# Kernel tuning notes

Measured on AMD Instinct MI355X. Metric: run time of the kernel, lower is better.

## Reference

```python
import jax, jax.numpy as jnp
import numpy as np
from jax import lax

K = 3
STRIDE = 1
PAD = 1
DIL = 1
EPS = 1e-5


def conv2d(x, w, b):
    y = lax.conv_general_dilated(
        x, w, (STRIDE, STRIDE), [(PAD, PAD), (PAD, PAD)],
        rhs_dilation=(DIL, DIL), dimension_numbers=('NCHW', 'OIHW', 'NCHW'))
    return y + b[None, :, None, None]


def deform_conv(x, offset, w):
    # x: [B,C,H,W], offset: [B,2*K2,Ho,Wo] (dy,dx interleaved per tap), w: [O,C,K,K]
    B, C, H, W = x.shape
    O = w.shape[0]
    K2 = K * K
    Ho, Wo = offset.shape[2], offset.shape[3]
    ky, kx = jnp.meshgrid(jnp.arange(K), jnp.arange(K), indexing='ij')
    # base sampling grid per kernel tap: [K2,Ho,Wo] (broadcast)
    by = (ky.reshape(K2, 1, 1) * DIL).astype(x.dtype) + (jnp.arange(Ho) * STRIDE - PAD).astype(x.dtype).reshape(1, Ho, 1)
    bx = (kx.reshape(K2, 1, 1) * DIL).astype(x.dtype) + (jnp.arange(Wo) * STRIDE - PAD).astype(x.dtype).reshape(1, 1, Wo)
    off = offset.reshape(B, K2, 2, Ho, Wo)
    py = by[None] + off[:, :, 0]  # [B,K2,Ho,Wo]
    px = bx[None] + off[:, :, 1]
    y0 = jnp.floor(py)
    x0 = jnp.floor(px)
    wy = py - y0
    wx = px - x0
    y0i = y0.astype(jnp.int32)
    x0i = x0.astype(jnp.int32)
    x_flat = x.reshape(B, C, H * W)

    def corner(yi, xi, cw):
        valid = ((yi >= 0) & (yi < H) & (xi >= 0) & (xi < W)).astype(x.dtype)
        idx = (jnp.clip(yi, 0, H - 1) * W + jnp.clip(xi, 0, W - 1)).reshape(B, -1)
        v = jax.vmap(lambda xb, ib: xb[:, ib])(x_flat, idx)  # [B,C,K2*Ho*Wo]
        return v * (cw * valid).reshape(B, 1, -1)

    val = (corner(y0i, x0i, (1 - wy) * (1 - wx))
           + corner(y0i, x0i + 1, (1 - wy) * wx)
           + corner(y0i + 1, x0i, wy * (1 - wx))
           + corner(y0i + 1, x0i + 1, wy * wx))  # [B,C,K2*Ho*Wo]
    samp = val.reshape(B, C, K2, Ho * Wo)
    out = jnp.einsum('bckp,ock->bop', samp, w.reshape(O, C, K2))
    return out.reshape(B, O, Ho, Wo)


def bn_gelu(x, gamma, beta):
    m = x.mean((0, 2, 3), keepdims=True)
    v = x.var((0, 2, 3), keepdims=True)
    xn = (x - m) / jnp.sqrt(v + EPS) * gamma[None, :, None, None] + beta[None, :, None, None]
    return jax.nn.gelu(xn, approximate=False)


def deform_block(x, w_off, b_off, w_def, gamma, beta):
    offset = conv2d(x, w_off, b_off)
    return bn_gelu(deform_conv(x, offset, w_def), gamma, beta)


def setup_inputs() -> dict:
    key = jax.random.key(0)
    ks = jax.random.split(key, 8)
    B, C, H, W = 4, 128, 112, 112
    fan = C * K * K
    x = jax.random.normal(ks[0], (B, C, H, W), jnp.float32)
    # offset conv weights: small random (original inits to 0; randomized to exercise sampling)
    w_off1 = jax.random.normal(ks[1], (2 * K * K, C, K, K), jnp.float32) * 0.01
    b_off1 = jnp.zeros((2 * K * K,), jnp.float32)
    w_def1 = jax.random.normal(ks[2], (C, C, K, K), jnp.float32) / np.sqrt(fan)
    gamma1 = jnp.ones((C,), jnp.float32)
    beta1 = jnp.zeros((C,), jnp.float32)
    w_off2 = jax.random.normal(ks[3], (2 * K * K, C, K, K), jnp.float32) * 0.01
    b_off2 = jnp.zeros((2 * K * K,), jnp.float32)
    w_def2 = jax.random.normal(ks[4], (C, C, K, K), jnp.float32) / np.sqrt(fan)
    gamma2 = jnp.ones((C,), jnp.float32)
    beta2 = jnp.zeros((C,), jnp.float32)
    return dict(x=x, w_off1=w_off1, b_off1=b_off1, w_def1=w_def1, gamma1=gamma1, beta1=beta1,
                w_off2=w_off2, b_off2=b_off2, w_def2=w_def2, gamma2=gamma2, beta2=beta2)


def reference(x, w_off1, b_off1, w_def1, gamma1, beta1,
              w_off2, b_off2, w_def2, gamma2, beta2):
    inp = x
    x = deform_block(x, w_off1, b_off1, w_def1, gamma1, beta1)
    x = deform_block(x, w_off2, b_off2, w_def2, gamma2, beta2)
    return x + inp
```

## Files before the change

kernel.cpp:

```cpp
#include <hip/hip_runtime.h>
#include <hip/hip_bf16.h>
#include <math.h>

#define HW 12544
#define CC 128
#define BB 4

typedef short bf16x8 __attribute__((ext_vector_type(8)));
typedef float f32x4 __attribute__((ext_vector_type(4)));

__device__ __forceinline__ float bf2f(unsigned int u) {
  union { unsigned int i; float f; } v; v.i = u << 16; return v.f;
}
__device__ __forceinline__ unsigned short f2bf(float f) {
  __hip_bfloat16 h = __float2bfloat16(f);
  return *reinterpret_cast<unsigned short*>(&h);
}
__device__ __forceinline__ float gelu(float v) {
  return 0.5f * v * (1.f + erff(v * 0.70710678118654752f));
}
__device__ __forceinline__ unsigned uc4(const uint4& v, int q) {
  return q == 0 ? v.x : q == 1 ? v.y : q == 2 ? v.z : v.w;
}

__global__ __launch_bounds__(256) void to_nhwc(const float* __restrict__ x,
                                               unsigned short* __restrict__ xh) {
  const int pt = blockIdx.x, ct = blockIdx.y, b = blockIdx.z;
  const int p0 = pt * 32, c0 = ct * 32;
  const int tid = threadIdx.x;
  __shared__ float ls[32][33];
  int col = tid & 31, r = tid >> 5;
#pragma unroll
  for (int i = 0; i < 4; i++) {
    int c = c0 + r + i * 8;
    ls[r + i * 8][col] = x[((size_t)(b * CC) + c) * HW + p0 + col];
  }
  __syncthreads();
  int px = tid >> 3, cq = (tid & 7) * 4;
  ushort4 v;
  v.x = f2bf(ls[cq + 0][px]);
  v.y = f2bf(ls[cq + 1][px]);
  v.z = f2bf(ls[cq + 2][px]);
  v.w = f2bf(ls[cq + 3][px]);
  *(ushort4*)&xh[((size_t)(b * HW) + p0 + px) * CC + c0 + cq] = v;
}

__global__ void pack_all(const float* __restrict__ wd1, const float* __restrict__ wo1,
                         const float* __restrict__ wd2, const float* __restrict__ wo2,
                         unsigned short* __restrict__ wpk1, unsigned short* __restrict__ wopk1,
                         unsigned short* __restrict__ wpk2, unsigned short* __restrict__ wopk2) {
  int i = blockIdx.x * 256 + threadIdx.x;
  if (i < 294912) {
    int ii = (i < 147456) ? i : i - 147456;
    const float* src = (i < 147456) ? wd1 : wd2;
    unsigned short* dst = (i < 147456) ? wpk1 : wpk2;
    int j = ii & 7, lane = (ii >> 3) & 63, ks = (ii >> 9) & 3, mo = (ii >> 11) & 7, k2 = ii >> 14;
    int o = mo * 16 + (lane & 15), c = ks * 32 + ((lane >> 4) << 3) + j;
    dst[ii] = f2bf(src[(o * CC + c) * 9 + k2]);
  } else {
    int ii = i - 294912;
    const float* src = (ii < 36864) ? wo1 : wo2;
    unsigned short* dst = (ii < 36864) ? wopk1 : wopk2;
    ii = (ii < 36864) ? ii : ii - 36864;
    int j = ii & 7, lane = (ii >> 3) & 63, ks = (ii >> 9) & 3, mo = (ii >> 11) & 1, k2 = ii >> 12;
    int o = mo * 16 + (lane & 15), c = ks * 32 + ((lane >> 4) << 3) + j;
    dst[ii] = (o < 18) ? f2bf(src[(o * CC + c) * 9 + k2]) : (unsigned short)0;
  }
}

__global__ __launch_bounds__(256) void offset_mfma(
    const unsigned short* __restrict__ xh, const unsigned short* __restrict__ wopk,
    const float* __restrict__ boff, float* __restrict__ offs2) {
  const int bid0 = blockIdx.x;
  const int bid = (bid0 & 7) * 98 + (bid0 >> 3);
  const int b = bid / 196;
  const int p0 = (bid % 196) * 64;
  const int tid = threadIdx.x;
  const int l = tid & 63, w = tid >> 6;
  const int hl = l & 15, ph = l >> 4;
  const int row = l & 15, grp = l >> 4;
  __shared__ unsigned short s_smp[2][8192];
  const unsigned short* xb = xh + (size_t)b * HW * CC + hl * 8;
  f32x4 acc[2];
  acc[0] = (f32x4){0.f, 0.f, 0.f, 0.f};
  acc[1] = (f32x4){0.f, 0.f, 0.f, 0.f};
  uint4 g2[4];
  bf16x8 af[2][4];

#define OISSUE(K2T)                                                            \
  {                                                                            \
    int ky = (K2T) / 3, kx = (K2T) % 3;                                        \
    _Pragma("unroll") for (int s = 0; s < 4; s++) {                            \
      int pxl = w * 16 + s * 4 + ph;                                           \
      int p = p0 + pxl;                                                        \
      int ho = p / 112, wo = p - ho * 112;                                     \
      int y = ho + ky - 1, x = wo + kx - 1;                                    \
      uint4 t = make_uint4(0u, 0u, 0u, 0u);                                    \
      if (((unsigned)y < 112u) & ((unsigned)x < 112u))                         \
        t = *(const uint4*)&xb[(size_t)(y * 112 + x) * CC];                    \
      g2[s] = t;                                                               \
    }                                                                          \
  }

#define OCOMMIT(BNBUF)                                                         \
  _Pragma("unroll") for (int s = 0; s < 4; s++) {                              \
    int pxl = w * 16 + s * 4 + ph;                                             \
    *(uint4*)((char*)&s_smp[BNBUF][0] +                                        \
              ((pxl * 256 + hl * 16) ^ ((pxl & 7) << 4))) = g2[s];             \
  }

#define OMFMA(BCBUF, ksB)                                                      \
  __builtin_amdgcn_s_setprio(1);                                               \
  _Pragma("unroll") for (int ks = ksB; ks < ksB + 2; ks++) {                   \
    int pxr = w * 16 + row;                                                    \
    bf16x8 bfr = *(const bf16x8*)((const char*)&s_smp[BCBUF][0] +              \
                 ((pxr * 256 + ks * 64 + grp * 16) ^ ((pxr & 7) << 4)));       \
    _Pragma("unroll") for (int m = 0; m < 2; m++)                              \
      acc[m] = __builtin_amdgcn_mfma_f32_16x16x32_bf16(af[m][ks], bfr, acc[m], 0, 0, 0); \
  }                                                                            \
  __builtin_amdgcn_s_setprio(0);

#define OLOADW(K2T)                                                            \
  {                                                                            \
    const unsigned short* wb = wopk + (size_t)(K2T) * 4096;                    \
    _Pragma("unroll") for (int m = 0; m < 2; m++)                              \
      _Pragma("unroll") for (int ks = 0; ks < 4; ks++)                         \
        af[m][ks] = *(const bf16x8*)&wb[(m * 4 + ks) * 512 + l * 8];           \
  }

#define OITER(K2T, BC, BN)                                                     \
  {                                                                            \
    if ((K2T) < 8) { OISSUE((K2T) + 1); }                                      \
    OMFMA(BC, 0);                                                              \
    if ((K2T) < 8) { OCOMMIT(BN); }                                            \
    OMFMA(BC, 2);                                                              \
    if ((K2T) < 8) { OLOADW((K2T) + 1); }                                      \
  }

  OISSUE(0); OCOMMIT(0); OLOADW(0);
  OITER(0, 0, 1) OITER(1, 1, 0) OITER(2, 0, 1) OITER(3, 1, 0) OITER(4, 0, 1)
  OITER(5, 1, 0) OITER(6, 0, 1) OITER(7, 1, 0) OITER(8, 0, 1)
#undef OISSUE
#undef OCOMMIT
#undef OMFMA
#undef OLOADW
#undef OITER

  int p = p0 + w * 16 + row;
  {
    float2 w0 = make_float2(acc[0][0] + boff[grp * 4 + 0], acc[0][1] + boff[grp * 4 + 1]);
    float2 w1 = make_float2(acc[0][2] + boff[grp * 4 + 2], acc[0][3] + boff[grp * 4 + 3]);
    *(float2*)&offs2[((size_t)(b * 9 + grp * 2) * HW + p) * 2] = w0;
    *(float2*)&offs2[((size_t)(b * 9 + grp * 2 + 1) * HW + p) * 2] = w1;
    if (grp == 0) {
      float2 w2 = make_float2(acc[1][0] + boff[16], acc[1][1] + boff[17]);
      *(float2*)&offs2[((size_t)(b * 9 + 8) * HW + p) * 2] = w2;
    }
  }
}

__global__ __launch_bounds__(256, 3) void deform_mfma(
    const unsigned short* __restrict__ xh, const float* __restrict__ offs2,
    const unsigned short* __restrict__ wpk, unsigned short* __restrict__ zh,
    float* __restrict__ part) {
  const int bid0 = blockIdx.x;
  const int bid = (bid0 & 7) * 196 + (bid0 >> 3);
  const int b = bid / 392;
  const int p0 = (bid % 392) * 32;
  const int tid = threadIdx.x;
  const int l = tid & 63, w = tid >> 6;
  const int hl = l & 15, ph = l >> 4;
  const int row = l & 15, grp = l >> 4;
  __shared__ unsigned short s_smp[2][4096];
  __shared__ uint4 s_coord[9][32];

  for (int e = tid; e < 288; e += 256) {
    int k2 = e >> 5, px = e & 31;
    int p = p0 + px;
    int ho = p / 112, wo = p - ho * 112;
    int ky = k2 / 3, kx = k2 - 3 * ky;
    float2 dv = *(const float2*)&offs2[((size_t)(b * 9 + k2) * HW + p) * 2];
    float py = (float)(ho + ky - 1) + dv.x;
    float pxf = (float)(wo + kx - 1) + dv.y;
    float y0f = floorf(py), x0f = floorf(pxf);
    float wy = py - y0f, wx = pxf - x0f;
    int y0 = (int)y0f, x0 = (int)x0f;
    int y1 = y0 + 1, x1 = x0 + 1;
    bool iy0 = ((unsigned)y0 < 112u), iy1 = ((unsigned)y1 < 112u);
    bool ix0 = ((unsigned)x0 < 112u), ix1 = ((unsigned)x1 < 112u);
    float v00 = (iy0 & ix0) ? (1.f - wy) * (1.f - wx) : 0.f;
    float v01 = (iy0 & ix1) ? (1.f - wy) * wx : 0.f;
    float v10 = (iy1 & ix0) ? wy * (1.f - wx) : 0.f;
    float v11 = (iy1 & ix1) ? wy * wx : 0.f;
    int y0c = min(max(y0, 0), 111), y1c = min(max(y1, 0), 111);
    int x0c = min(max(x0, 0), 111), x1c = min(max(x1, 0), 111);
    uint4 ce;
    ce.x = (unsigned)(y0c * 112 + x0c) | ((unsigned)(y0c * 112 + x1c) << 16);
    ce.y = (unsigned)(y1c * 112 + x0c) | ((unsigned)(y1c * 112 + x1c) << 16);
    ce.z = (unsigned)f2bf(v00) | ((unsigned)f2bf(v01) << 16);
    ce.w = (unsigned)f2bf(v10) | ((unsigned)f2bf(v11) << 16);
    s_coord[k2][px] = ce;
  }

  const unsigned short* xb = xh + (size_t)b * HW * CC + hl * 8;
  f32x4 acc[2][2];
#pragma unroll
  for (int m = 0; m < 2; m++)
#pragma unroll
    for (int n = 0; n < 2; n++) acc[m][n] = (f32x4){0.f, 0.f, 0.f, 0.f};
  uint4 g[2][4];
  uint2 wts[2];
  bf16x8 af[2][4];
  __syncthreads();

#define DISSUE(K2T)                                                            \
  _Pragma("unroll") for (int s = 0; s < 2; s++) {                              \
    int pxl = w * 8 + s * 4 + ph;                                              \
    uint4 cc = s_coord[K2T][pxl];                                              \
    wts[s] = make_uint2(cc.z, cc.w);                                           \
    g[s][0] = *(const uint4*)&xb[(size_t)(cc.x & 0xffffu) * CC];               \
    g[s][1] = *(const uint4*)&xb[(size_t)(cc.x >> 16) * CC];                   \
    g[s][2] = *(const uint4*)&xb[(size_t)(cc.y & 0xffffu) * CC];               \
    g[s][3] = *(const uint4*)&xb[(size_t)(cc.y >> 16) * CC];                   \
  }

#define DCOMMIT(BNBUF)                                                         \
  _Pragma("unroll") for (int s = 0; s < 2; s++) {                              \
    int pxl = w * 8 + s * 4 + ph;                                              \
    float w00 = bf2f(wts[s].x & 0xffffu), w01 = bf2f(wts[s].x >> 16);          \
    float w10 = bf2f(wts[s].y & 0xffffu), w11 = bf2f(wts[s].y >> 16);          \
    unsigned rr[4];                                                            \
    _Pragma("unroll") for (int q = 0; q < 4; q++) {                            \
      unsigned a0 = uc4(g[s][0], q), a1 = uc4(g[s][1], q);                     \
      unsigned a2 = uc4(g[s][2], q), a3 = uc4(g[s][3], q);                     \
      float elo = w00 * bf2f(a0 & 0xffffu) + w01 * bf2f(a1 & 0xffffu)          \
                + w10 * bf2f(a2 & 0xffffu) + w11 * bf2f(a3 & 0xffffu);         \
      float ehi = w00 * bf2f(a0 >> 16) + w01 * bf2f(a1 >> 16)                  \
                + w10 * bf2f(a2 >> 16) + w11 * bf2f(a3 >> 16);                 \
      rr[q] = (unsigned)f2bf(elo) | ((unsigned)f2bf(ehi) << 16);               \
    }                                                                          \
    *(uint4*)((char*)&s_smp[BNBUF][0] +                                        \
              ((pxl * 256 + hl * 16) ^ ((pxl & 7) << 4))) =                    \
        make_uint4(rr[0], rr[1], rr[2], rr[3]);                                \
  }

#define DMFMA(BCBUF, ksB)                                                      \
  __builtin_amdgcn_s_setprio(1);                                               \
  _Pragma("unroll") for (int ks = ksB; ks < ksB + 2; ks++) {                   \
    bf16x8 bfr[2];                                                             \
    _Pragma("unroll") for (int n = 0; n < 2; n++) {                            \
      int pxr = n * 16 + row;                                                  \
      bfr[n] = *(const bf16x8*)((const char*)&s_smp[BCBUF][0] +                \
               ((pxr * 256 + ks * 64 + grp * 16) ^ ((pxr & 7) << 4)));         \
    }                                                                          \
    _Pragma("unroll") for (int m = 0; m < 2; m++)                              \
      _Pragma("unroll") for (int n = 0; n < 2; n++)                            \
        acc[m][n] = __builtin_amdgcn_mfma_f32_16x16x32_bf16(af[m][ks], bfr[n], acc[m][n], 0, 0, 0); \
  }                                                                            \
  __builtin_amdgcn_s_setprio(0);

#define DLOADW(K2T)                                                            \
  {                                                                            \
    const unsigned short* wb = wpk + (size_t)((K2T) * 8 + w * 2) * 2048;       \
    _Pragma("unroll") for (int m = 0; m < 2; m++)                              \
      _Pragma("unroll") for (int ks = 0; ks < 4; ks++)                         \
        af[m][ks] = *(const bf16x8*)&wb[(m * 4 + ks) * 512 + l * 8];           \
  }

#define DITER(K2T, BC, BN)                                                     \
  {                                                                            \
    if ((K2T) < 8) { DISSUE((K2T) + 1); }                                      \
    DMFMA(BC, 0);                                                              \
    if ((K2T) < 8) { DCOMMIT(BN); }                                            \
    DMFMA(BC, 2);                                                              \
    if ((K2T) < 8) { DLOADW((K2T) + 1); __syncthreads(); }                     \
  }

  DISSUE(0); DCOMMIT(0); DLOADW(0);
  __syncthreads();
  DITER(0, 0, 1) DITER(1, 1, 0) DITER(2, 0, 1) DITER(3, 1, 0) DITER(4, 0, 1)
  DITER(5, 1, 0) DITER(6, 0, 1) DITER(7, 1, 0) DITER(8, 0, 1)
#undef DISSUE
#undef DCOMMIT
#undef DMFMA
#undef DLOADW
#undef DITER

#pragma unroll
  for (int m = 0; m < 2; m++)
#pragma unroll
    for (int n = 0; n < 2; n++) {
      int o = (w * 2 + m) * 16 + grp * 4;
      size_t px = (size_t)(b * HW) + p0 + n * 16 + row;
      unsigned lo = (unsigned)f2bf(acc[m][n][0]) | ((unsigned)f2bf(acc[m][n][1]) << 16);
      unsigned hi = (unsigned)f2bf(acc[m][n][2]) | ((unsigned)f2bf(acc[m][n][3]) << 16);
      *(uint2*)&zh[px * CC + o] = make_uint2(lo, hi);
    }

  float sv[8], qv[8];
#pragma unroll
  for (int m = 0; m < 2; m++)
#pragma unroll
    for (int r = 0; r < 4; r++) {
      float s = 0.f, q = 0.f;
#pragma unroll
      for (int n = 0; n < 2; n++) { float v = acc[m][n][r]; s += v; q += v * v; }
      sv[m * 4 + r] = s; qv[m * 4 + r] = q;
    }
#pragma unroll
  for (int d = 1; d < 16; d <<= 1)
#pragma unroll
    for (int i = 0; i < 8; i++) {
      sv[i] += __shfl_xor(sv[i], d);
      qv[i] += __shfl_xor(qv[i], d);
    }
  if (row == 0) {
#pragma unroll
    for (int m = 0; m < 2; m++)
#pragma unroll
      for (int r = 0; r < 4; r++) {
        int ch = (w * 2 + m) * 16 + grp * 4 + r;
        part[(size_t)ch * 1568 + bid] = sv[m * 4 + r];
        part[(size_t)(128 + ch) * 1568 + bid] = qv[m * 4 + r];
      }
  }
}

__global__ __launch_bounds__(256) void bn_fin(const float* __restrict__ part,
                                              const float* __restrict__ gamma,
                                              const float* __restrict__ beta,
                                              float* __restrict__ stats) {
  const int c = blockIdx.x, t = threadIdx.x;
  float s = 0.f, q = 0.f;
  for (int j = t; j < 1568; j += 256) {
    s += part[(size_t)c * 1568 + j];
    q += part[(size_t)(128 + c) * 1568 + j];
  }
  __shared__ float ss[256], sq2[256];
  ss[t] = s; sq2[t] = q;
  __syncthreads();
  for (int d = 128; d > 0; d >>= 1) {
    if (t < d) { ss[t] += ss[t + d]; sq2[t] += sq2[t + d]; }
    __syncthreads();
  }
  if (t == 0) {
    float N = 50176.f;
    float m = ss[0] / N;
    float var = sq2[0] / N - m * m;
    stats[c] = m;
    stats[128 + c] = rsqrtf(var + 1e-5f) * gamma[c];
    stats[256 + c] = beta[c];
  }
}

__global__ __launch_bounds__(256) void bn_gelu_to_bf16(
    const unsigned short* __restrict__ zh, const float* __restrict__ stats,
    unsigned short* __restrict__ yh) {
  int i = blockIdx.x * 256 + threadIdx.x;
  int c0 = (i & 15) * 8;
  uint4 zv = ((const uint4*)zh)[i];
  f32x4 m0 = *(const f32x4*)&stats[c0], m1 = *(const f32x4*)&stats[c0 + 4];
  f32x4 r0 = *(const f32x4*)&stats[128 + c0], r1 = *(const f32x4*)&stats[128 + c0 + 4];
  f32x4 b0 = *(const f32x4*)&stats[256 + c0], b1 = *(const f32x4*)&stats[256 + c0 + 4];
  float v[8] = {bf2f(zv.x & 0xffffu), bf2f(zv.x >> 16), bf2f(zv.y & 0xffffu), bf2f(zv.y >> 16),
                bf2f(zv.z & 0xffffu), bf2f(zv.z >> 16), bf2f(zv.w & 0xffffu), bf2f(zv.w >> 16)};
  unsigned o[4];
#pragma unroll
  for (int j = 0; j < 4; j++) {
    float mj0 = (j < 2) ? m0[j * 2] : m1[j * 2 - 4], mj1 = (j < 2) ? m0[j * 2 + 1] : m1[j * 2 - 3];
    float rj0 = (j < 2) ? r0[j * 2] : r1[j * 2 - 4], rj1 = (j < 2) ? r0[j * 2 + 1] : r1[j * 2 - 3];
    float bj0 = (j < 2) ? b0[j * 2] : b1[j * 2 - 4], bj1 = (j < 2) ? b0[j * 2 + 1] : b1[j * 2 - 3];
    float e0 = gelu((v[j * 2] - mj0) * rj0 + bj0);
    float e1 = gelu((v[j * 2 + 1] - mj1) * rj1 + bj1);
    o[j] = (unsigned)f2bf(e0) | ((unsigned)f2bf(e1) << 16);
  }
  ((uint4*)yh)[i] = make_uint4(o[0], o[1], o[2], o[3]);
}

__global__ __launch_bounds__(256) void bn_gelu_final(
    const unsigned short* __restrict__ zh, const float* __restrict__ stats,
    const float* __restrict__ x, float* __restrict__ out) {
  const int pt = blockIdx.x, b = blockIdx.y;
  const int p0 = pt * 16;
  const int tid = threadIdx.x;
  __shared__ float ls[16][129];
  {
    int cq = tid & 15, r = tid >> 4;
    uint4 zv = *(const uint4*)&zh[((size_t)(b * HW) + p0 + r) * CC + cq * 8];
    float v[8] = {bf2f(zv.x & 0xffffu), bf2f(zv.x >> 16), bf2f(zv.y & 0xffffu), bf2f(zv.y >> 16),
                  bf2f(zv.z & 0xffffu), bf2f(zv.z >> 16), bf2f(zv.w & 0xffffu), bf2f(zv.w >> 16)};
    f32x4 m0 = *(const f32x4*)&stats[cq * 8], m1 = *(const f32x4*)&stats[cq * 8 + 4];
    f32x4 r0 = *(const f32x4*)&stats[128 + cq * 8], r1 = *(const f32x4*)&stats[128 + cq * 8 + 4];
    f32x4 b0 = *(const f32x4*)&stats[256 + cq * 8], b1 = *(const f32x4*)&stats[256 + cq * 8 + 4];
#pragma unroll
    for (int j = 0; j < 4; j++) {
      ls[r][cq * 8 + j] = gelu((v[j] - m0[j]) * r0[j] + b0[j]);
      ls[r][cq * 8 + 4 + j] = gelu((v[4 + j] - m1[j]) * r1[j] + b1[j]);
    }
  }
  __syncthreads();
  int c = tid & 127, half = tid >> 7;
  const float* xr = x + ((size_t)(b * CC) + c) * HW + p0 + half * 8;
  float* orow = out + ((size_t)(b * CC) + c) * HW + p0 + half * 8;
  float4 o1 = make_float4(ls[half * 8 + 0][c], ls[half * 8 + 1][c],
                          ls[half * 8 + 2][c], ls[half * 8 + 3][c]);
  float4 o2 = make_float4(ls[half * 8 + 4][c], ls[half * 8 + 5][c],
                          ls[half * 8 + 6][c], ls[half * 8 + 7][c]);
  float4 x1 = *(const float4*)&xr[0];
  float4 x2 = *(const float4*)&xr[4];
  o1.x += x1.x; o1.y += x1.y; o1.z += x1.z; o1.w += x1.w;
  o2.x += x2.x; o2.y += x2.y; o2.z += x2.z; o2.w += x2.w;
  *(float4*)&orow[0] = o1;
  *(float4*)&orow[4] = o2;
}

extern "C" void kernel_launch(void* const* d_in, const int* in_sizes, int n_in,
                              void* d_out, int out_size, void* d_ws, size_t ws_size,
                              hipStream_t stream) {
  const float* x = (const float*)d_in[0];
  const float* w_off1 = (const float*)d_in[1];
  const float* b_off1 = (const float*)d_in[2];
  const float* w_def1 = (const float*)d_in[3];
  const float* gamma1 = (const float*)d_in[4];
  const float* beta1 = (const float*)d_in[5];
  const float* w_off2 = (const float*)d_in[6];
  const float* b_off2 = (const float*)d_in[7];
  const float* w_def2 = (const float*)d_in[8];
  const float* gamma2 = (const float*)d_in[9];
  const float* beta2 = (const float*)d_in[10];
  float* out = (float*)d_out;

  char* ws = (char*)d_ws;
  unsigned short* xhb = (unsigned short*)ws;
  unsigned short* zhb = (unsigned short*)(ws + 12845056);
  float* offb = (float*)(ws + 25690112);
  unsigned short* wpk1 = (unsigned short*)(ws + 29302784);
  unsigned short* wpk2 = (unsigned short*)(ws + 29597696);
  unsigned short* wopk1 = (unsigned short*)(ws + 29892608);
  unsigned short* wopk2 = (unsigned short*)(ws + 29966336);
  float* partb = (float*)(ws + 30040064);
  float* statsb = (float*)(ws + 31645696);

  to_nhwc<<<dim3(392, 4, 4), 256, 0, stream>>>(x, xhb);
  pack_all<<<1440, 256, 0, stream>>>(w_def1, w_off1, w_def2, w_off2,
                                     wpk1, wopk1, wpk2, wopk2);

  offset_mfma<<<784, 256, 0, stream>>>(xhb, wopk1, b_off1, offb);
  deform_mfma<<<1568, 256, 0, stream>>>(xhb, offb, wpk1, zhb, partb);
  bn_fin<<<128, 256, 0, stream>>>(partb, gamma1, beta1, statsb);
  bn_gelu_to_bf16<<<3136, 256, 0, stream>>>(zhb, statsb, xhb);

  offset_mfma<<<784, 256, 0, stream>>>(xhb, wopk2, b_off2, offb);
  deform_mfma<<<1568, 256, 0, stream>>>(xhb, offb, wpk2, zhb, partb);
  bn_fin<<<128, 256, 0, stream>>>(partb, gamma2, beta2, statsb);
  bn_gelu_final<<<dim3(784, 4), 256, 0, stream>>>(zhb, statsb, x, out);
}
```

Measured before the change: 177.4 us.

## Split offset conv work across waves by output-channel half with smaller pixel tiles

The offset convolution kernel now uses 32-pixel tiles instead of 64 and launches twice as many blocks. Within a block, pairs of waves share a 16-pixel group and split the two 16-row output-channel MFMA tiles between them. This halves shared memory, registers and gather loads per wave, which should raise occupancy and parallelism. In exchange it adds a block barrier per tap, since waves now read samples staged by other waves, and one wave of each pair does little useful work (only 2 of its 16 output channels are real).

```diff
diff --git a/kernel.cpp b/kernel.cpp
--- a/kernel.cpp
+++ b/kernel.cpp
@@ -72,26 +72,26 @@
     const unsigned short* __restrict__ xh, const unsigned short* __restrict__ wopk,
     const float* __restrict__ boff, float* __restrict__ offs2) {
   const int bid0 = blockIdx.x;
-  const int bid = (bid0 & 7) * 98 + (bid0 >> 3);
-  const int b = bid / 196;
-  const int p0 = (bid % 196) * 64;
+  const int bid = (bid0 & 7) * 196 + (bid0 >> 3);
+  const int b = bid / 392;
+  const int p0 = (bid % 392) * 32;
   const int tid = threadIdx.x;
   const int l = tid & 63, w = tid >> 6;
   const int hl = l & 15, ph = l >> 4;
   const int row = l & 15, grp = l >> 4;
-  __shared__ unsigned short s_smp[2][8192];
+  const int pxg = (w >> 1) * 16;
+  const int mw = w & 1;
+  __shared__ unsigned short s_smp[2][4096];
   const unsigned short* xb = xh + (size_t)b * HW * CC + hl * 8;
-  f32x4 acc[2];
-  acc[0] = (f32x4){0.f, 0.f, 0.f, 0.f};
-  acc[1] = (f32x4){0.f, 0.f, 0.f, 0.f};
-  uint4 g2[4];
-  bf16x8 af[2][4];
+  f32x4 acc = (f32x4){0.f, 0.f, 0.f, 0.f};
+  uint4 g2[2];
+  bf16x8 af[4];
 
 #define OISSUE(K2T)                                                            \
   {                                                                            \
     int ky = (K2T) / 3, kx = (K2T) % 3;                                        \
-    _Pragma("unroll") for (int s = 0; s < 4; s++) {                            \
-      int pxl = w * 16 + s * 4 + ph;                                           \
+    _Pragma("unroll") for (int s = 0; s < 2; s++) {                            \
+      int pxl = w * 8 + s * 4 + ph;                                            \
       int p = p0 + pxl;                                                        \
       int ho = p / 112, wo = p - ho * 112;                                     \
       int y = ho + ky - 1, x = wo + kx - 1;                                    \
@@ -103,8 +103,8 @@
   }
 
 #define OCOMMIT(BNBUF)                                                         \
-  _Pragma("unroll") for (int s = 0; s < 4; s++) {                              \
-    int pxl = w * 16 + s * 4 + ph;                                             \
+  _Pragma("unroll") for (int s = 0; s < 2; s++) {                              \
+    int pxl = w * 8 + s * 4 + ph;                                              \
     *(uint4*)((char*)&s_smp[BNBUF][0] +                                        \
               ((pxl * 256 + hl * 16) ^ ((pxl & 7) << 4))) = g2[s];             \
   }
@@ -112,20 +112,18 @@
 #define OMFMA(BCBUF, ksB)                                                      \
   __builtin_amdgcn_s_setprio(1);                                               \
   _Pragma("unroll") for (int ks = ksB; ks < ksB + 2; ks++) {                   \
-    int pxr = w * 16 + row;                                                    \
+    int pxr = pxg + row;                                                       \
     bf16x8 bfr = *(const bf16x8*)((const char*)&s_smp[BCBUF][0] +              \
                  ((pxr * 256 + ks * 64 + grp * 16) ^ ((pxr & 7) << 4)));       \
-    _Pragma("unroll") for (int m = 0; m < 2; m++)                              \
-      acc[m] = __builtin_amdgcn_mfma_f32_16x16x32_bf16(af[m][ks], bfr, acc[m], 0, 0, 0); \
+    acc = __builtin_amdgcn_mfma_f32_16x16x32_bf16(af[ks], bfr, acc, 0, 0, 0);  \
   }                                                                            \
   __builtin_amdgcn_s_setprio(0);
 
 #define OLOADW(K2T)                                                            \
   {                                                                            \
     const unsigned short* wb = wopk + (size_t)(K2T) * 4096;                    \
-    _Pragma("unroll") for (int m = 0; m < 2; m++)                              \
-      _Pragma("unroll") for (int ks = 0; ks < 4; ks++)                         \
-        af[m][ks] = *(const bf16x8*)&wb[(m * 4 + ks) * 512 + l * 8];           \
+    _Pragma("unroll") for (int ks = 0; ks < 4; ks++)                           \
+      af[ks] = *(const bf16x8*)&wb[(mw * 4 + ks) * 512 + l * 8];               \
   }
 
 #define OITER(K2T, BC, BN)                                                     \
@@ -134,10 +132,11 @@
     OMFMA(BC, 0);                                                              \
     if ((K2T) < 8) { OCOMMIT(BN); }                                            \
     OMFMA(BC, 2);                                                              \
-    if ((K2T) < 8) { OLOADW((K2T) + 1); }                                      \
+    if ((K2T) < 8) { OLOADW((K2T) + 1); __syncthreads(); }                     \
   }
 
   OISSUE(0); OCOMMIT(0); OLOADW(0);
+  __syncthreads();
   OITER(0, 0, 1) OITER(1, 1, 0) OITER(2, 0, 1) OITER(3, 1, 0) OITER(4, 0, 1)
   OITER(5, 1, 0) OITER(6, 0, 1) OITER(7, 1, 0) OITER(8, 0, 1)
 #undef OISSUE
@@ -146,16 +145,15 @@
 #undef OLOADW
 #undef OITER
 
-  int p = p0 + w * 16 + row;
-  {
-    float2 w0 = make_float2(acc[0][0] + boff[grp * 4 + 0], acc[0][1] + boff[grp * 4 + 1]);
-    float2 w1 = make_float2(acc[0][2] + boff[grp * 4 + 2], acc[0][3] + boff[grp * 4 + 3]);
+  int p = p0 + pxg + row;
+  if (mw == 0) {
+    float2 w0 = make_float2(acc[0] + boff[grp * 4 + 0], acc[1] + boff[grp * 4 + 1]);
+    float2 w1 = make_float2(acc[2] + boff[grp * 4 + 2], acc[3] + boff[grp * 4 + 3]);
     *(float2*)&offs2[((size_t)(b * 9 + grp * 2) * HW + p) * 2] = w0;
     *(float2*)&offs2[((size_t)(b * 9 + grp * 2 + 1) * HW + p) * 2] = w1;
-    if (grp == 0) {
-      float2 w2 = make_float2(acc[1][0] + boff[16], acc[1][1] + boff[17]);
-      *(float2*)&offs2[((size_t)(b * 9 + 8) * HW + p) * 2] = w2;
-    }
+  } else if (grp == 0) {
+    float2 w2 = make_float2(acc[0] + boff[16], acc[1] + boff[17]);
+    *(float2*)&offs2[((size_t)(b * 9 + 8) * HW + p) * 2] = w2;
   }
 }
 
@@ -445,12 +443,12 @@
   pack_all<<<1440, 256, 0, stream>>>(w_def1, w_off1, w_def2, w_off2,
                                      wpk1, wopk1, wpk2, wopk2);
 
-  offset_mfma<<<784, 256, 0, stream>>>(xhb, wopk1, b_off1, offb);
+  offset_mfma<<<1568, 256, 0, stream>>>(xhb, wopk1, b_off1, offb);
   deform_mfma<<<1568, 256, 0, stream>>>(xhb, offb, wpk1, zhb, partb);
   bn_fin<<<128, 256, 0, stream>>>(partb, gamma1, beta1, statsb);
   bn_gelu_to_bf16<<<3136, 256, 0, stream>>>(zhb, statsb, xhb);
 
-  offset_mfma<<<784, 256, 0, stream>>>(xhb, wopk2, b_off2, offb);
+  offset_mfma<<<1568, 256, 0, stream>>>(xhb, wopk2, b_off2, offb);
   deform_mfma<<<1568, 256, 0, stream>>>(xhb, offb, wpk2, zhb, partb);
   bn_fin<<<128, 256, 0, stream>>>(partb, gamma2, beta2, statsb);
   bn_gelu_final<<<dim3(784, 4), 256, 0, stream>>>(zhb, statsb, x, out);
```

Result: faster. 172.5 us (-2.7%).
